# Performance work log

Measured on AMD Instinct MI355X. Metric: run time of the kernel, lower is better.

## Reference

```python
import math
import jax, jax.numpy as jnp
import numpy as np

EPS = 1e-5
B, S, D = 2, 2048, 2048
Z, HD, H, N = 512, 4096, 8, 8
ZH, VH = Z // H, HD // H  # 64, 512
GROUPS = 32


def timestep_norm(x, w, b):
    # cumulative (over time) group normalization; groups of dg channels
    dg = D // GROUPS
    xg = x.reshape(B, S, GROUPS, dg)
    s1 = jnp.cumsum(xg.sum(-1), axis=1)                 # [B,S,G]
    s2 = jnp.cumsum(jnp.square(xg).sum(-1), axis=1)     # [B,S,G]
    cnt = (jnp.arange(S, dtype=x.dtype) + 1.0) * dg
    mean = s1 / cnt[None, :, None]
    var = s2 / cnt[None, :, None] - jnp.square(mean)
    xn = (xg - mean[..., None]) * jax.lax.rsqrt(var[..., None] + EPS)
    return xn.reshape(B, S, D) * w + b


def cema(x, alpha, delta, theta, gamma, omega):
    # complex multi-head EMA: h_t = a*e^{i\theta} x_t + (1-a*d)*e^{i\theta} h_{t-1};
    # y_t = Re(gamma^H h_t) + omega * x_t    (real-arithmetic form, scan over time)
    p = jax.nn.sigmoid(alpha)                      # [D,N]
    qm = 1.0 - p * jax.nn.sigmoid(delta)           # [D,N]
    phase = jax.nn.sigmoid(theta)[:, None] * (2.0 * math.pi * (jnp.arange(N, dtype=x.dtype) + 1.0) / N)
    c, s = jnp.cos(phase), jnp.sin(phase)
    ur, ui = p * c, p * s
    qr, qi = qm * c, qm * s
    gr, gi = gamma[..., 0], gamma[..., 1]

    def step(h, xt):  # xt: [B,D]
        hr, hi = h
        nhr = qr * hr - qi * hi + ur * xt[..., None]
        nhi = qi * hr + qr * hi + ui * xt[..., None]
        y = jnp.sum(nhr * gr + nhi * gi, axis=-1)  # [B,D]
        return (nhr, nhi), y

    h0 = (jnp.zeros((B, D, N), x.dtype), jnp.zeros((B, D, N), x.dtype))
    _, ys = jax.lax.scan(step, h0, jnp.moveaxis(x, 1, 0))
    return jnp.moveaxis(ys, 0, 1) + x * omega


def rmsnorm(x, w=None):
    y = x * jax.lax.rsqrt(jnp.mean(jnp.square(x), axis=-1, keepdims=True) + EPS)
    return y if w is None else y * w


def apply_rotary(xq, xk, freqs):
    # xq/xk: [B,S,H,ZH]; freqs: [S, ZH//2, 2] (cos, sin)
    cos = freqs[None, :, None, :, 0]
    sin = freqs[None, :, None, :, 1]

    def rot(x):
        xr = x.reshape(*x.shape[:-1], ZH // 2, 2)
        re, im = xr[..., 0], xr[..., 1]
        out = jnp.stack([re * cos - im * sin, re * sin + im * cos], axis=-1)
        return out.reshape(x.shape)

    return rot(xq), rot(xk)


def setup_inputs():
    key = jax.random.key(0)
    ks = jax.random.split(key, 24)
    p = 0.02
    inp = {
        "x": jax.random.normal(ks[0], (B, S, D), jnp.float32),
        "tn_weight": 1.0 + p * jax.random.normal(ks[1], (D,), jnp.float32),
        "tn_bias": p * jax.random.normal(ks[2], (D,), jnp.float32),
        "ema_alpha": jax.random.normal(ks[3], (D, N), jnp.float32),
        "ema_delta": jax.random.normal(ks[4], (D, N), jnp.float32),
        "ema_theta": jax.random.normal(ks[5], (D,), jnp.float32),
        "ema_gamma": jax.random.normal(ks[6], (D, N, 2), jnp.float32) / math.sqrt(N),
        "ema_omega": p * jax.random.normal(ks[7], (D,), jnp.float32),
        "rms_weight": 1.0 + p * jax.random.normal(ks[8], (D,), jnp.float32),
        "wz_w": jax.random.normal(ks[9], (D, Z), jnp.float32) / math.sqrt(D),
        "wz_b": p * jax.random.normal(ks[10], (Z,), jnp.float32),
        "wv_w": jax.random.normal(ks[11], (D, HD), jnp.float32) / math.sqrt(D),
        "wv_b": p * jax.random.normal(ks[12], (HD,), jnp.float32),
        "wr_w": jax.random.normal(ks[13], (D, HD), jnp.float32) / math.sqrt(D),
        "wr_b": p * jax.random.normal(ks[14], (HD,), jnp.float32),
        "wh1_w": jax.random.normal(ks[15], (D, D), jnp.float32) / math.sqrt(D),
        "wh1_b": p * jax.random.normal(ks[16], (D,), jnp.float32),
        "wh2_w": jax.random.normal(ks[17], (HD, D), jnp.float32) / math.sqrt(HD),
        "attn_gamma": p * jax.random.normal(ks[18], (2, Z), jnp.float32),
        "attn_beta": p * jax.random.normal(ks[19], (2, Z), jnp.float32),
    }
    # rotary freqs (cos, sin) for head dim ZH
    inv = 1.0 / (10000.0 ** (np.arange(0, ZH, 2, dtype=np.float32) / ZH))
    ang = np.arange(S, dtype=np.float32)[:, None] * inv[None, :]
    inp["freqs_cis"] = jnp.asarray(np.stack([np.cos(ang), np.sin(ang)], axis=-1))
    return inp


def reference(x, freqs_cis, tn_weight, tn_bias, ema_alpha, ema_delta, ema_theta,
              ema_gamma, ema_omega, rms_weight, wz_w, wz_b, wv_w, wv_b, wr_w, wr_b,
              wh1_w, wh1_b, wh2_w, attn_gamma, attn_beta):
    residual = x
    out_tsn = timestep_norm(x, tn_weight, tn_bias)
    out_cema = cema(out_tsn, ema_alpha, ema_delta, ema_theta, ema_gamma, ema_omega)
    mx = rmsnorm(out_cema, rms_weight)

    z = mx @ wz_w + wz_b                              # [B,S,Z]
    z = rmsnorm(z.reshape(B, S, H, ZH)).reshape(B, S, Z)
    gamma = (attn_gamma + 1.0) / math.sqrt(ZH)        # [2,Z]
    z2 = z[:, :, None, :] * gamma + attn_beta         # [B,S,2,Z]
    q, k = z2[:, :, 0], z2[:, :, 1]

    v = jax.nn.silu(out_tsn @ wv_w + wv_b)            # [B,S,HD]
    r = jax.nn.silu(mx @ wr_w + wr_b)                 # [B,S,HD]

    qh = q.reshape(B, S, H, ZH)
    kh = k.reshape(B, S, H, ZH)
    vh = v.reshape(B, S, H, VH)
    qh, kh = apply_rotary(qh, kh, freqs_cis)

    # causal additive mask; scale 1.0 (folded into gamma)
    neg = jnp.finfo(jnp.float32).min
    mask = jnp.where(jnp.tril(jnp.ones((S, S), bool)), 0.0, neg).astype(jnp.float32)
    scores = jnp.einsum('bqhd,bkhd->bhqk', qh, kh) + mask
    probs = jax.nn.softmax(scores.astype(jnp.float32), axis=-1).astype(qh.dtype)
    attn = jnp.einsum('bhqk,bkhd->bqhd', probs, vh).reshape(B, S, HD)

    attn = attn * r
    h = (mx @ wh1_w + wh1_b) + attn @ wh2_w
    return h + residual
```

## Files before the change

### kernel.cpp

```cpp
#include <hip/hip_runtime.h>
#include <stdint.h>


typedef __bf16 bf16_t;
typedef bf16_t bf16x8 __attribute__((ext_vector_type(8)));
typedef float floatx4 __attribute__((ext_vector_type(4)));
typedef __attribute__((address_space(1))) unsigned int as1_uint;
typedef __attribute__((address_space(3))) unsigned int as3_uint;

static constexpr int kB = 2, kS = 2048, kD = 2048;
static constexpr int kZ = 512, kHD = 4096, kH = 8;
static constexpr int kG = 32;
static constexpr int kC = 64, kL = 32;

__device__ __forceinline__ void async16(void* lds, const void* g) {
  __builtin_amdgcn_global_load_lds((const as1_uint*)(size_t)g, (as3_uint*)lds, 16, 0, 0);
}

__device__ __forceinline__ float sigm(float x) { return 1.0f / (1.0f + expf(-x)); }

__global__ __launch_bounds__(256) void wtrans_kernel(const float* __restrict__ W,
                                                     bf16_t* __restrict__ Wt,
                                                     int K, int N, int ldWt,
                                                     int colOff) {
  __shared__ float tile[32][33];
  int n0 = blockIdx.x * 32, k0 = blockIdx.y * 32;
  int tx = threadIdx.x & 31, ty = threadIdx.x >> 5;
#pragma unroll
  for (int i = 0; i < 32; i += 8)
    tile[ty + i][tx] = W[(size_t)(k0 + ty + i) * N + n0 + tx];
  __syncthreads();
#pragma unroll
  for (int i = 0; i < 32; i += 8)
    Wt[(size_t)(n0 + ty + i) * ldWt + colOff + k0 + tx] = (bf16_t)tile[tx][ty + i];
}

__global__ __launch_bounds__(256) void tsn_sums(const float* __restrict__ x,
                                                float* __restrict__ g1,
                                                float* __restrict__ g2) {
  int bs = blockIdx.x, t = threadIdx.x;
  const float4* rp = (const float4*)(x + (size_t)bs * kD + t * 8);
  float4 a = rp[0], b = rp[1];
  float s1 = a.x + a.y + a.z + a.w + b.x + b.y + b.z + b.w;
  float s2 = a.x * a.x + a.y * a.y + a.z * a.z + a.w * a.w +
             b.x * b.x + b.y * b.y + b.z * b.z + b.w * b.w;
  s1 += __shfl_xor(s1, 1); s2 += __shfl_xor(s2, 1);
  s1 += __shfl_xor(s1, 2); s2 += __shfl_xor(s2, 2);
  s1 += __shfl_xor(s1, 4); s2 += __shfl_xor(s2, 4);
  if ((t & 7) == 0) {
    int g = t >> 3, b_ = bs >> 11, s = bs & 2047;
    size_t idx = ((size_t)b_ * kG + g) * kS + s;
    g1[idx] = s1; g2[idx] = s2;
  }
}

__global__ void tsn_scan(float* __restrict__ g1, float* __restrict__ g2) {
  int lane = threadIdx.x;
  size_t base = (size_t)blockIdx.x * kS;
  float c1 = 0.f, c2 = 0.f;
  for (int c = 0; c < kS / 64; ++c) {
    size_t idx = base + c * 64 + lane;
    float v1 = g1[idx], v2 = g2[idx];
#pragma unroll
    for (int off = 1; off < 64; off <<= 1) {
      float t1 = __shfl_up(v1, off), t2 = __shfl_up(v2, off);
      if (lane >= off) { v1 += t1; v2 += t2; }
    }
    v1 += c1; v2 += c2;
    g1[idx] = v1; g2[idx] = v2;
    c1 = __shfl(v1, 63); c2 = __shfl(v2, 63);
  }
}

__global__ __launch_bounds__(256) void tsn_norm(const float* __restrict__ x,
    const float* __restrict__ g1, const float* __restrict__ g2,
    const float* __restrict__ w, const float* __restrict__ bias,
    float* __restrict__ tsn, bf16_t* __restrict__ tsnb) {
  int bs = blockIdx.x, t = threadIdx.x;
  int b = bs >> 11, s = bs & 2047, g = t >> 3;
  float cnt = (float)(s + 1) * 64.0f;
  size_t gidx = ((size_t)b * kG + g) * kS + s;
  float mean = g1[gidx] / cnt;
  float inv = rsqrtf(g2[gidx] / cnt - mean * mean + 1e-5f);
  size_t base = (size_t)bs * kD + t * 8;
  float4 a = ((const float4*)(x + base))[0];
  float4 c = ((const float4*)(x + base))[1];
  float v[8] = {a.x, a.y, a.z, a.w, c.x, c.y, c.z, c.w};
  float4 w0 = ((const float4*)(w + t * 8))[0], w1 = ((const float4*)(w + t * 8))[1];
  float4 b0 = ((const float4*)(bias + t * 8))[0], b1 = ((const float4*)(bias + t * 8))[1];
  float wv[8] = {w0.x, w0.y, w0.z, w0.w, w1.x, w1.y, w1.z, w1.w};
  float bv[8] = {b0.x, b0.y, b0.z, b0.w, b1.x, b1.y, b1.z, b1.w};
  float r[8];
  bf16x8 ob;
#pragma unroll
  for (int i = 0; i < 8; ++i) {
    r[i] = (v[i] - mean) * inv * wv[i] + bv[i];
    ob[i] = (bf16_t)r[i];
  }
  ((float4*)(tsn + base))[0] = make_float4(r[0], r[1], r[2], r[3]);
  ((float4*)(tsn + base))[1] = make_float4(r[4], r[5], r[6], r[7]);
  *(bf16x8*)(tsnb + base) = ob;
}

__device__ __forceinline__ void cema_coeffs(const float* __restrict__ alpha,
    const float* __restrict__ delta, float st, int d,
    float (&qr)[8], float (&qi)[8], float (&ur)[8], float (&ui)[8]) {
  const float4* ap = (const float4*)(alpha + (size_t)d * 8);
  const float4* dp = (const float4*)(delta + (size_t)d * 8);
  float4 a0 = ap[0], a1 = ap[1], d0 = dp[0], d1 = dp[1];
  float av[8] = {a0.x, a0.y, a0.z, a0.w, a1.x, a1.y, a1.z, a1.w};
  float dv[8] = {d0.x, d0.y, d0.z, d0.w, d1.x, d1.y, d1.z, d1.w};
#pragma unroll
  for (int n = 0; n < 8; ++n) {
    float p = sigm(av[n]);
    float qm = 1.0f - p * sigm(dv[n]);
    float ph = st * (0.78539816339744831f * (float)(n + 1));
    float cs = cosf(ph), sn = sinf(ph);
    qr[n] = qm * cs; qi[n] = qm * sn;
    ur[n] = p * cs;  ui[n] = p * sn;
  }
}

__global__ __launch_bounds__(256) void cema_pass1(const float* __restrict__ tsn,
    const float* __restrict__ alpha, const float* __restrict__ delta,
    const float* __restrict__ theta, float2* __restrict__ hend) {
  int b = blockIdx.x >> 6, c = blockIdx.x & 63;
  int d = blockIdx.y * 256 + threadIdx.x;
  float st = sigm(theta[d]);
  float qr[8], qi[8], ur[8], ui[8];
  cema_coeffs(alpha, delta, st, d, qr, qi, ur, ui);
  float hr[8] = {0}, hi[8] = {0};
  const float* xp = tsn + ((size_t)b * kS + c * kL) * kD + d;
  for (int i = 0; i < kL; ++i) {
    float xt = xp[(size_t)i * kD];
#pragma unroll
    for (int n = 0; n < 8; ++n) {
      float tr = fmaf(qr[n], hr[n], fmaf(-qi[n], hi[n], ur[n] * xt));
      float ti = fmaf(qi[n], hr[n], fmaf(qr[n], hi[n], ui[n] * xt));
      hr[n] = tr; hi[n] = ti;
    }
  }
  float2* op = hend + (((size_t)(b * kC + c)) * kD + d) * 8;
#pragma unroll
  for (int n = 0; n < 8; ++n) op[n] = make_float2(hr[n], hi[n]);
}

__global__ __launch_bounds__(256) void cema_pass2(const float2* __restrict__ hend,
    const float* __restrict__ alpha, const float* __restrict__ delta,
    const float* __restrict__ theta, float2* __restrict__ hinit) {
  int tid = blockIdx.x * 256 + threadIdx.x;
  int n = tid & 7, d = (tid >> 3) & 2047, b = tid >> 14;
  int dn = d * 8 + n;
  float p = sigm(alpha[dn]);
  float qm = 1.0f - p * sigm(delta[dn]);
  float ph = sigm(theta[d]) * (0.78539816339744831f * (float)(n + 1));
  float ar = qm * cosf(ph), ai = qm * sinf(ph);
#pragma unroll
  for (int t = 0; t < 5; ++t) {
    float nr = ar * ar - ai * ai;
    ai = 2.0f * ar * ai;
    ar = nr;
  }
  float hr = 0.f, hi = 0.f;
  for (int c = 0; c < kC; ++c) {
    size_t idx = (((size_t)(b * kC + c)) * kD + d) * 8 + n;
    hinit[idx] = make_float2(hr, hi);
    float2 e = hend[idx];
    float nr = fmaf(ar, hr, fmaf(-ai, hi, e.x));
    float ni = fmaf(ai, hr, fmaf(ar, hi, e.y));
    hr = nr; hi = ni;
  }
}

__global__ __launch_bounds__(256) void cema_pass3(const float* __restrict__ tsn,
    const float* __restrict__ alpha, const float* __restrict__ delta,
    const float* __restrict__ theta, const float* __restrict__ gamma,
    const float* __restrict__ omega, const float2* __restrict__ hinit,
    float* __restrict__ outc) {
  int b = blockIdx.x >> 6, c = blockIdx.x & 63;
  int d = blockIdx.y * 256 + threadIdx.x;
  float st = sigm(theta[d]);
  float qr[8], qi[8], ur[8], ui[8];
  cema_coeffs(alpha, delta, st, d, qr, qi, ur, ui);
  float gr[8], gi[8];
  const float4* gp = (const float4*)(gamma + (size_t)d * 16);
#pragma unroll
  for (int m = 0; m < 4; ++m) {
    float4 g = gp[m];
    gr[m * 2] = g.x; gi[m * 2] = g.y; gr[m * 2 + 1] = g.z; gi[m * 2 + 1] = g.w;
  }
  float om = omega[d];
  float hr[8], hi[8];
  const float2* ip = hinit + (((size_t)(b * kC + c)) * kD + d) * 8;
#pragma unroll
  for (int n = 0; n < 8; ++n) { float2 h = ip[n]; hr[n] = h.x; hi[n] = h.y; }
  const float* xp = tsn + ((size_t)b * kS + c * kL) * kD + d;
  float* op = outc + ((size_t)b * kS + c * kL) * kD + d;
  for (int i = 0; i < kL; ++i) {
    float xt = xp[(size_t)i * kD];
    float y = 0.f;
#pragma unroll
    for (int n = 0; n < 8; ++n) {
      float tr = fmaf(qr[n], hr[n], fmaf(-qi[n], hi[n], ur[n] * xt));
      float ti = fmaf(qi[n], hr[n], fmaf(qr[n], hi[n], ui[n] * xt));
      hr[n] = tr; hi[n] = ti;
      y = fmaf(tr, gr[n], fmaf(ti, gi[n], y));
    }
    op[(size_t)i * kD] = fmaf(xt, om, y);
  }
}

__global__ __launch_bounds__(256) void rms_kernel(const float* __restrict__ in,
                                                  const float* __restrict__ w,
                                                  bf16_t* __restrict__ outb) {
  int bs = blockIdx.x, t = threadIdx.x;
  size_t base = (size_t)bs * kD + t * 8;
  float4 a = ((const float4*)(in + base))[0];
  float4 c = ((const float4*)(in + base))[1];
  float v[8] = {a.x, a.y, a.z, a.w, c.x, c.y, c.z, c.w};
  float ss = 0.f;
#pragma unroll
  for (int i = 0; i < 8; ++i) ss += v[i] * v[i];
#pragma unroll
  for (int off = 1; off < 64; off <<= 1) ss += __shfl_xor(ss, off);
  __shared__ float red[4];
  if ((t & 63) == 0) red[t >> 6] = ss;
  __syncthreads();
  ss = red[0] + red[1] + red[2] + red[3];
  float inv = rsqrtf(ss * (1.0f / 2048.0f) + 1e-5f);
  float4 w0 = ((const float4*)(w + t * 8))[0], w1 = ((const float4*)(w + t * 8))[1];
  float wv[8] = {w0.x, w0.y, w0.z, w0.w, w1.x, w1.y, w1.z, w1.w};
  bf16x8 ob;
#pragma unroll
  for (int i = 0; i < 8; ++i) ob[i] = (bf16_t)(v[i] * inv * wv[i]);
  *(bf16x8*)(outb + base) = ob;
}

__global__ __launch_bounds__(256) void zpost_kernel(const float* __restrict__ z,
    const float* __restrict__ ag, const float* __restrict__ ab,
    const float* __restrict__ freqs, bf16_t* __restrict__ q, bf16_t* __restrict__ k) {
  int bs = blockIdx.x, t = threadIdx.x;
  int b = bs >> 11, s = bs & 2047;
  int h = t >> 5, i = t & 31;
  const float* zr = z + (size_t)bs * kZ + h * 64;
  float re = zr[2 * i], im = zr[2 * i + 1];
  float ss = re * re + im * im;
#pragma unroll
  for (int off = 1; off < 32; off <<= 1) ss += __shfl_xor(ss, off);
  float inv = rsqrtf(ss * (1.0f / 64.0f) + 1e-5f);
  float zne = re * inv, zno = im * inv;
  const float rs = 0.125f;
  int ze = h * 64 + 2 * i, zo = ze + 1;
  float qe = zne * ((ag[ze] + 1.f) * rs) + ab[ze];
  float qo = zno * ((ag[zo] + 1.f) * rs) + ab[zo];
  float ke = zne * ((ag[kZ + ze] + 1.f) * rs) + ab[kZ + ze];
  float ko = zno * ((ag[kZ + zo] + 1.f) * rs) + ab[kZ + zo];
  float cs = freqs[((size_t)s * 32 + i) * 2 + 0];
  float sn = freqs[((size_t)s * 32 + i) * 2 + 1];
  size_t o = (((size_t)b * kH + h) * kS + s) * 64 + 2 * i;
  q[o]     = (bf16_t)(qe * cs - qo * sn);
  q[o + 1] = (bf16_t)(qe * sn + qo * cs);
  k[o]     = (bf16_t)(ke * cs - ko * sn);
  k[o + 1] = (bf16_t)(ke * sn + ko * cs);
}

__global__ __launch_bounds__(256) void gemm_fused3(
    const bf16_t* __restrict__ tsnb, const bf16_t* __restrict__ mx,
    const bf16_t* __restrict__ wvT, const bf16_t* __restrict__ wrT,
    const bf16_t* __restrict__ wzT, const float* __restrict__ wv_b,
    const float* __restrict__ wr_b, const float* __restrict__ wz_b,
    bf16_t* __restrict__ vTb, bf16_t* __restrict__ rb,
    float* __restrict__ zbuf) {
  __shared__ __align__(16) bf16_t sA[2][128 * 32];
  __shared__ __align__(16) bf16_t sB[2][128 * 32];
  const int bid = blockIdx.x;
  const bf16_t* A; const bf16_t* Bt; const float* bias;
  int N, epi, sub;
  if (bid < 1024)      { sub = bid;        A = tsnb; Bt = wvT; bias = wv_b; N = kHD; epi = 1; }
  else if (bid < 2048) { sub = bid - 1024; A = mx;   Bt = wrT; bias = wr_b; N = kHD; epi = 2; }
  else                 { sub = bid - 2048; A = mx;   Bt = wzT; bias = wz_b; N = kZ;  epi = 0; }
  const int m0 = (sub & 31) * 128, n0 = (sub >> 5) * 128;
  const int t = threadIdx.x;
  const int wave = t >> 6, lane = t & 63;
  const int quad = lane >> 4, l16 = lane & 15;
  const int wm = (wave >> 1) * 64, wn = (wave & 1) * 64;
  const int K = kD;

  floatx4 acc[4][4];
#pragma unroll
  for (int i = 0; i < 4; ++i)
#pragma unroll
    for (int j = 0; j < 4; ++j) acc[i][j] = (floatx4){0.f, 0.f, 0.f, 0.f};

  const int seg0 = wave * 64 + lane;
  const int seg1 = 256 + wave * 64 + lane;
  const int r0 = seg0 >> 2, c0 = (seg0 & 3) * 8;
  const int r1 = seg1 >> 2, c1 = (seg1 & 3) * 8;

  auto stage = [&](int buf, int kt) {
    async16(sA[buf] + (size_t)(wave * 64) * 8,       A + (size_t)(m0 + r0) * K + kt + c0);
    async16(sA[buf] + (size_t)(256 + wave * 64) * 8, A + (size_t)(m0 + r1) * K + kt + c1);
    async16(sB[buf] + (size_t)(wave * 64) * 8,       Bt + (size_t)(n0 + r0) * K + kt + c0);
    async16(sB[buf] + (size_t)(256 + wave * 64) * 8, Bt + (size_t)(n0 + r1) * K + kt + c1);
  };

  stage(0, 0);
  __syncthreads();

  const int nsteps = K >> 5;
  for (int st = 0; st < nsteps; ++st) {
    const int cur = st & 1;
    if (st + 1 < nsteps) stage(cur ^ 1, (st + 1) << 5);

    bf16x8 af[4], bfr[4];
#pragma unroll
    for (int i = 0; i < 4; ++i)
      af[i] = *(const bf16x8*)(sA[cur] + (wm + i * 16 + l16) * 32 + quad * 8);
#pragma unroll
    for (int j = 0; j < 4; ++j)
      bfr[j] = *(const bf16x8*)(sB[cur] + (wn + j * 16 + l16) * 32 + quad * 8);
#pragma unroll
    for (int i = 0; i < 4; ++i)
#pragma unroll
      for (int j = 0; j < 4; ++j)
        acc[i][j] = __builtin_amdgcn_mfma_f32_16x16x32_bf16(af[i], bfr[j], acc[i][j], 0, 0, 0);

    __syncthreads();
  }

#pragma unroll
  for (int i = 0; i < 4; ++i) {
#pragma unroll
    for (int j = 0; j < 4; ++j) {
#pragma unroll
      for (int r = 0; r < 4; ++r) {
        int row = m0 + wm + i * 16 + quad * 4 + r;
        int col = n0 + wn + j * 16 + l16;
        size_t idx = (size_t)row * N + col;
        float v = acc[i][j][r];
        if (epi == 0) {
          zbuf[idx] = v + bias[col];
        } else if (epi == 1) {
          v += bias[col];
          v = v / (1.f + __expf(-v));
          size_t vidx = ((size_t)(row >> 11) * kHD + col) * (size_t)kS + (row & 2047);
          vTb[vidx] = (bf16_t)v;
        } else {
          v += bias[col];
          v = v / (1.f + __expf(-v));
          rb[idx] = (bf16_t)v;
        }
      }
    }
  }
}

__global__ __launch_bounds__(256) void gemm_bt(const bf16_t* __restrict__ A1,
    int lda1, const bf16_t* __restrict__ A2, int lda2, int K1,
    const bf16_t* __restrict__ Bt, int M, int N, int K,
    const float* __restrict__ bias, const float* __restrict__ add1,
    float* __restrict__ outF) {
  __shared__ __align__(16) bf16_t sA[2][128 * 32];
  __shared__ __align__(16) bf16_t sB[2][128 * 32];
  const int t = threadIdx.x;
  const int wave = t >> 6, lane = t & 63;
  const int quad = lane >> 4, l16 = lane & 15;
  const int m0 = blockIdx.x * 128, n0 = blockIdx.y * 128;
  const int wm = (wave >> 1) * 64, wn = (wave & 1) * 64;

  floatx4 acc[4][4];
#pragma unroll
  for (int i = 0; i < 4; ++i)
#pragma unroll
    for (int j = 0; j < 4; ++j) acc[i][j] = (floatx4){0.f, 0.f, 0.f, 0.f};

  const int seg0 = wave * 64 + lane;
  const int seg1 = 256 + wave * 64 + lane;
  const int r0 = seg0 >> 2, c0 = (seg0 & 3) * 8;
  const int r1 = seg1 >> 2, c1 = (seg1 & 3) * 8;

  auto stage = [&](int buf, int kt) {
    const bf16_t* Ab; int ldab; int kk;
    if (kt < K1) { Ab = A1; ldab = lda1; kk = kt; }
    else         { Ab = A2; ldab = lda2; kk = kt - K1; }
    async16(sA[buf] + (size_t)(wave * 64) * 8,       Ab + (size_t)(m0 + r0) * ldab + kk + c0);
    async16(sA[buf] + (size_t)(256 + wave * 64) * 8, Ab + (size_t)(m0 + r1) * ldab + kk + c1);
    async16(sB[buf] + (size_t)(wave * 64) * 8,       Bt + (size_t)(n0 + r0) * K + kt + c0);
    async16(sB[buf] + (size_t)(256 + wave * 64) * 8, Bt + (size_t)(n0 + r1) * K + kt + c1);
  };

  stage(0, 0);
  __syncthreads();

  const int nsteps = K >> 5;
  for (int st = 0; st < nsteps; ++st) {
    const int cur = st & 1;
    if (st + 1 < nsteps) stage(cur ^ 1, (st + 1) << 5);

    bf16x8 af[4], bfr[4];
#pragma unroll
    for (int i = 0; i < 4; ++i)
      af[i] = *(const bf16x8*)(sA[cur] + (wm + i * 16 + l16) * 32 + quad * 8);
#pragma unroll
    for (int j = 0; j < 4; ++j)
      bfr[j] = *(const bf16x8*)(sB[cur] + (wn + j * 16 + l16) * 32 + quad * 8);
#pragma unroll
    for (int i = 0; i < 4; ++i)
#pragma unroll
      for (int j = 0; j < 4; ++j)
        acc[i][j] = __builtin_amdgcn_mfma_f32_16x16x32_bf16(af[i], bfr[j], acc[i][j], 0, 0, 0);

    __syncthreads();
  }

#pragma unroll
  for (int i = 0; i < 4; ++i) {
#pragma unroll
    for (int j = 0; j < 4; ++j) {
#pragma unroll
      for (int r = 0; r < 4; ++r) {
        int row = m0 + wm + i * 16 + quad * 4 + r;
        int col = n0 + wn + j * 16 + l16;
        size_t idx = (size_t)row * N + col;
        outF[idx] = acc[i][j][r] + bias[col] + add1[idx];
      }
    }
  }
}

__global__ __launch_bounds__(256) void attn_kernel(const bf16_t* __restrict__ qg,
    const bf16_t* __restrict__ kg, const bf16_t* __restrict__ vT,
    const bf16_t* __restrict__ rg, bf16_t* __restrict__ attnG) {
  const int bid = blockIdx.x;
  const int qt = (kS / 64 - 1) - (bid >> 5);
  const int bh = (bid >> 1) & 15;
  const int vs = bid & 1;
  const int b = bh >> 3, h = bh & 7;
  const int t = threadIdx.x;
  const int w = t >> 6, lane = t & 63;
  const int quad = lane >> 4, l16 = lane & 15;
  const int q0 = qt * 64;

  __shared__ __align__(16) bf16_t sP[2][64 * 64];
  __shared__ __align__(16) bf16_t sK[2][64 * 64];
  __shared__ float sM[64], sL[64], sAl[2][64];
  if (t < 64) { sM[t] = 0.f; sL[t] = 0.f; }

  const bf16_t* qbase = qg + ((size_t)bh * kS + q0) * 64;
  const bf16_t* kbase = kg + (size_t)bh * kS * 64;
  const bf16_t* vbase = vT + ((size_t)bh * 512 + vs * 256 + w * 64) * kS;

  auto stage_k = [&](bf16_t* dstbuf, int k0) {
#pragma unroll
    for (int half = 0; half < 2; ++half) {
      int seg = half * 256 + w * 64 + lane;
      int r = seg >> 3, cc = seg & 7;
      async16(dstbuf + (size_t)(half * 256 + w * 64) * 8,
              kbase + (size_t)(k0 + r) * 64 + (cc ^ (r & 7)) * 8);
    }
  };

  bf16x8 qfrag[2];
#pragma unroll
  for (int ks = 0; ks < 2; ++ks)
    qfrag[ks] = *(const bf16x8*)(qbase + (size_t)(w * 16 + l16) * 64 + ks * 32 + quad * 8);

  floatx4 oacc[4][4];
#pragma unroll
  for (int i = 0; i < 4; ++i)
#pragma unroll
    for (int j = 0; j < 4; ++j) oacc[i][j] = (floatx4){0.f, 0.f, 0.f, 0.f};

  stage_k(sK[0], 0);
  __syncthreads();

  for (int kt = 0; kt <= qt; ++kt) {
    const int k0 = kt * 64;
    const int pb = kt & 1;

    if (kt < qt) stage_k(sK[pb ^ 1], k0 + 64);

    bf16x8 vf[2][4];
#pragma unroll
    for (int ks = 0; ks < 2; ++ks)
#pragma unroll
      for (int nj = 0; nj < 4; ++nj)
        vf[ks][nj] = *(const bf16x8*)(vbase + (size_t)(nj * 16 + l16) * kS + k0 + ks * 32 + quad * 8);

    floatx4 sacc[4];
#pragma unroll
    for (int nt = 0; nt < 4; ++nt) sacc[nt] = (floatx4){0.f, 0.f, 0.f, 0.f};
#pragma unroll
    for (int ks = 0; ks < 2; ++ks)
#pragma unroll
      for (int nt = 0; nt < 4; ++nt) {
        int row = nt * 16 + l16;
        int ch = (ks * 4 + quad) ^ (row & 7);
        bf16x8 kf = *(const bf16x8*)(sK[pb] + row * 64 + ch * 8);
        sacc[nt] = __builtin_amdgcn_mfma_f32_16x16x32_bf16(qfrag[ks], kf, sacc[nt], 0, 0, 0);
      }
    if (kt == qt) {
#pragma unroll
      for (int nt = 0; nt < 4; ++nt)
#pragma unroll
        for (int r = 0; r < 4; ++r) {
          int sk = k0 + nt * 16 + l16;
          int qq = q0 + w * 16 + quad * 4 + r;
          if (sk > qq) sacc[nt][r] = -1e30f;
        }
    }

    float mo[4], mloc[4], lspec[4];
#pragma unroll
    for (int r = 0; r < 4; ++r) {
      mo[r] = sM[w * 16 + quad * 4 + r];
      mloc[r] = fmaxf(fmaxf(sacc[0][r], sacc[1][r]), fmaxf(sacc[2][r], sacc[3][r]));
    }
#pragma unroll
    for (int r = 0; r < 4; ++r) {
      float s = 0.f;
#pragma unroll
      for (int nt = 0; nt < 4; ++nt) {
        float e = __expf(sacc[nt][r] - mo[r]);
        sacc[nt][r] = e;
        s += e;
      }
      lspec[r] = s;
    }
#pragma unroll
    for (int off = 1; off < 16; off <<= 1)
#pragma unroll
      for (int r = 0; r < 4; ++r) {
        mloc[r] = fmaxf(mloc[r], __shfl_xor(mloc[r], off));
        lspec[r] += __shfl_xor(lspec[r], off);
      }
    float mnew[4], al[4];
#pragma unroll
    for (int r = 0; r < 4; ++r) {
      mnew[r] = fmaxf(mo[r], mloc[r]);
      al[r] = __expf(mo[r] - mnew[r]);
    }
    if (l16 == 0) {
#pragma unroll
      for (int r = 0; r < 4; ++r) {
        int row = w * 16 + quad * 4 + r;
        sM[row] = mnew[r];
        sL[row] = al[r] * (sL[row] + lspec[r]);
        sAl[pb][row] = al[r];
      }
    }
#pragma unroll
    for (int nt = 0; nt < 4; ++nt)
#pragma unroll
      for (int r = 0; r < 4; ++r) {
        int row = w * 16 + quad * 4 + r;
        sP[pb][row * 64 + ((nt * 16 + l16) ^ ((row & 7) << 3))] = (bf16_t)(sacc[nt][r] * al[r]);
      }

    __syncthreads();

#pragma unroll
    for (int mi = 0; mi < 4; ++mi)
#pragma unroll
      for (int r = 0; r < 4; ++r) {
        float a = sAl[pb][mi * 16 + quad * 4 + r];
#pragma unroll
        for (int nj = 0; nj < 4; ++nj) oacc[mi][nj][r] *= a;
      }
    __builtin_amdgcn_s_setprio(1);
#pragma unroll
    for (int ks = 0; ks < 2; ++ks) {
      bf16x8 pa[4];
#pragma unroll
      for (int mi = 0; mi < 4; ++mi) {
        int row = mi * 16 + l16;
        pa[mi] = *(const bf16x8*)(sP[pb] + row * 64 + ((ks * 32 + quad * 8) ^ ((row & 7) << 3)));
      }
#pragma unroll
      for (int nj = 0; nj < 4; ++nj)
#pragma unroll
        for (int mi = 0; mi < 4; ++mi)
          oacc[mi][nj] = __builtin_amdgcn_mfma_f32_16x16x32_bf16(pa[mi], vf[ks][nj], oacc[mi][nj], 0, 0, 0);
    }
    __builtin_amdgcn_s_setprio(0);
  }

#pragma unroll
  for (int mi = 0; mi < 4; ++mi)
#pragma unroll
    for (int r = 0; r < 4; ++r) {
      int srow = q0 + mi * 16 + quad * 4 + r;
      float linv = 1.0f / sL[mi * 16 + quad * 4 + r];
#pragma unroll
      for (int nj = 0; nj < 4; ++nj) {
        int hd = h * 512 + vs * 256 + w * 64 + nj * 16 + l16;
        size_t idx = ((size_t)b * kS + srow) * kHD + hd;
        float rv = (float)rg[idx];
        attnG[idx] = (bf16_t)(oacc[mi][nj][r] * linv * rv);
      }
    }
}

extern "C" void kernel_launch(void* const* d_in, const int* in_sizes, int n_in,
                              void* d_out, int out_size, void* d_ws, size_t ws_size,
                              hipStream_t stream) {
  const float* x      = (const float*)d_in[0];
  const float* tnw    = (const float*)d_in[1];
  const float* tnb    = (const float*)d_in[2];
  const float* ealpha = (const float*)d_in[3];
  const float* edelta = (const float*)d_in[4];
  const float* etheta = (const float*)d_in[5];
  const float* egamma = (const float*)d_in[6];
  const float* eomega = (const float*)d_in[7];
  const float* rmsw   = (const float*)d_in[8];
  const float* wz_w   = (const float*)d_in[9];
  const float* wz_b   = (const float*)d_in[10];
  const float* wv_w   = (const float*)d_in[11];
  const float* wv_b   = (const float*)d_in[12];
  const float* wr_w   = (const float*)d_in[13];
  const float* wr_b   = (const float*)d_in[14];
  const float* wh1_w  = (const float*)d_in[15];
  const float* wh1_b  = (const float*)d_in[16];
  const float* wh2_w  = (const float*)d_in[17];
  const float* ag     = (const float*)d_in[18];
  const float* ab     = (const float*)d_in[19];
  const float* freqs  = (const float*)d_in[20];
  float* out = (float*)d_out;

  char* ws = (char*)d_ws;
  size_t off = 0;
  auto alloc = [&](size_t bytes) -> void* {
    void* p = ws + off;
    off += (bytes + 255) & ~(size_t)255;
    return p;
  };
  float*  tsn  = (float*)alloc(8388608ull * 4);
  bf16_t* tsnb = (bf16_t*)alloc(8388608ull * 2);
  float*  g1   = (float*)alloc(131072ull * 4);
  float*  g2   = (float*)alloc(131072ull * 4);
  float*  cema = (float*)alloc(8388608ull * 4);
  bf16_t* mx   = (bf16_t*)alloc(8388608ull * 2);
  bf16_t* wzT  = (bf16_t*)alloc(1048576ull * 2);
  bf16_t* wvT  = (bf16_t*)alloc(8388608ull * 2);
  bf16_t* wrT  = (bf16_t*)alloc(8388608ull * 2);
  bf16_t* whcT = (bf16_t*)alloc(12582912ull * 2);
  float*  zbuf = (float*)alloc(2097152ull * 4);
  bf16_t* qb   = (bf16_t*)alloc(2097152ull * 2);
  bf16_t* kb   = (bf16_t*)alloc(2097152ull * 2);
  bf16_t* rb   = (bf16_t*)alloc(16777216ull * 2);
  bf16_t* aG   = (bf16_t*)alloc(16777216ull * 2);
  bf16_t* vTb  = (bf16_t*)tsn;
  float*  h1   = cema;
  float2* hend  = (float2*)rb;
  float2* hinit = (float2*)aG;
  (void)h1;

  wtrans_kernel<<<dim3(kZ / 32, kD / 32), 256, 0, stream>>>(wz_w, wzT, kD, kZ, kD, 0);
  wtrans_kernel<<<dim3(kHD / 32, kD / 32), 256, 0, stream>>>(wv_w, wvT, kD, kHD, kD, 0);
  wtrans_kernel<<<dim3(kHD / 32, kD / 32), 256, 0, stream>>>(wr_w, wrT, kD, kHD, kD, 0);
  wtrans_kernel<<<dim3(kD / 32, kD / 32), 256, 0, stream>>>(wh1_w, whcT, kD, kD, 6144, 0);
  wtrans_kernel<<<dim3(kD / 32, kHD / 32), 256, 0, stream>>>(wh2_w, whcT, kHD, kD, 6144, kD);

  tsn_sums<<<kB * kS, 256, 0, stream>>>(x, g1, g2);
  tsn_scan<<<kB * kG, 64, 0, stream>>>(g1, g2);
  tsn_norm<<<kB * kS, 256, 0, stream>>>(x, g1, g2, tnw, tnb, tsn, tsnb);

  cema_pass1<<<dim3(kB * kC, kD / 256), 256, 0, stream>>>(tsn, ealpha, edelta,
                                                          etheta, hend);
  cema_pass2<<<kB * kD * 8 / 256, 256, 0, stream>>>(hend, ealpha, edelta,
                                                    etheta, hinit);
  cema_pass3<<<dim3(kB * kC, kD / 256), 256, 0, stream>>>(tsn, ealpha, edelta,
      etheta, egamma, eomega, hinit, cema);
  rms_kernel<<<kB * kS, 256, 0, stream>>>(cema, rmsw, mx);

  const int M = kB * kS;
  gemm_fused3<<<dim3(2176), 256, 0, stream>>>(tsnb, mx, wvT, wrT, wzT,
      wv_b, wr_b, wz_b, vTb, rb, zbuf);
  zpost_kernel<<<kB * kS, 256, 0, stream>>>(zbuf, ag, ab, freqs, qb, kb);
  attn_kernel<<<dim3(1024), 256, 0, stream>>>(qb, kb, vTb, rb, aG);
  gemm_bt<<<dim3(M / 128, kD / 128), 256, 0, stream>>>(mx, kD, aG, kHD, kD,
      whcT, M, kD, 6144, wh1_b, x, out);
  (void)in_sizes; (void)n_in; (void)out_size; (void)ws_size;
}
```

Measured before the change: 872.4 us.

## Overlap mx@wh1 GEMM with attention by co-launching in one kernel

The final GEMM is split in two. The independent mx@wh1 part (K=2048), plus bias and residual, now runs as 512 extra blocks appended to the attention launch, so it fills idle CUs while the causally imbalanced attention blocks run. A second GEMM over the attention output (K=4096) then adds onto the stored partial. This costs an extra fp32 write and read of the partial buffer and a separate launch for the second GEMM.

```diff
diff --git a/kernel.cpp b/kernel.cpp
--- a/kernel.cpp
+++ b/kernel.cpp
@@ -355,10 +355,254 @@
   }
 }
 
-__global__ __launch_bounds__(256) void gemm_bt(const bf16_t* __restrict__ A1,
-    int lda1, const bf16_t* __restrict__ A2, int lda2, int K1,
-    const bf16_t* __restrict__ Bt, int M, int N, int K,
-    const float* __restrict__ bias, const float* __restrict__ add1,
+__global__ __launch_bounds__(256) void fused_attn_wh1(
+    const bf16_t* __restrict__ qg, const bf16_t* __restrict__ kg,
+    const bf16_t* __restrict__ vT, const bf16_t* __restrict__ rg,
+    bf16_t* __restrict__ attnG,
+    const bf16_t* __restrict__ mx, const bf16_t* __restrict__ whcT,
+    const float* __restrict__ wh1_b, const float* __restrict__ x,
+    float* __restrict__ Pw0) {
+  __shared__ __align__(16) char smem[33792];
+  const int bid = blockIdx.x;
+  const int t = threadIdx.x;
+  const int w = t >> 6, lane = t & 63;
+  const int quad = lane >> 4, l16 = lane & 15;
+
+  if (bid >= 1024) {
+    bf16_t* sA = (bf16_t*)smem;
+    bf16_t* sB = (bf16_t*)(smem + 16384);
+    const int sub = bid - 1024;
+    const int m0 = (sub & 31) * 128, n0 = (sub >> 5) * 128;
+    const int wm = (w >> 1) * 64, wn = (w & 1) * 64;
+    const int N = kD, K = kD, ldB = 6144;
+
+    floatx4 acc[4][4];
+#pragma unroll
+    for (int i = 0; i < 4; ++i)
+#pragma unroll
+      for (int j = 0; j < 4; ++j) acc[i][j] = (floatx4){0.f, 0.f, 0.f, 0.f};
+
+    const int seg0 = w * 64 + lane;
+    const int seg1 = 256 + w * 64 + lane;
+    const int r0 = seg0 >> 2, c0 = (seg0 & 3) * 8;
+    const int r1 = seg1 >> 2, c1 = (seg1 & 3) * 8;
+
+    auto stage = [&](int buf, int kt) {
+      bf16_t* sAb = sA + buf * 4096;
+      bf16_t* sBb = sB + buf * 4096;
+      async16(sAb + (size_t)(w * 64) * 8,       mx + (size_t)(m0 + r0) * K + kt + c0);
+      async16(sAb + (size_t)(256 + w * 64) * 8, mx + (size_t)(m0 + r1) * K + kt + c1);
+      async16(sBb + (size_t)(w * 64) * 8,       whcT + (size_t)(n0 + r0) * ldB + kt + c0);
+      async16(sBb + (size_t)(256 + w * 64) * 8, whcT + (size_t)(n0 + r1) * ldB + kt + c1);
+    };
+
+    stage(0, 0);
+    __syncthreads();
+
+    const int nsteps = K >> 5;
+    for (int st = 0; st < nsteps; ++st) {
+      const int cur = st & 1;
+      if (st + 1 < nsteps) stage(cur ^ 1, (st + 1) << 5);
+
+      bf16x8 af[4], bfr[4];
+#pragma unroll
+      for (int i = 0; i < 4; ++i)
+        af[i] = *(const bf16x8*)(sA + cur * 4096 + (wm + i * 16 + l16) * 32 + quad * 8);
+#pragma unroll
+      for (int j = 0; j < 4; ++j)
+        bfr[j] = *(const bf16x8*)(sB + cur * 4096 + (wn + j * 16 + l16) * 32 + quad * 8);
+#pragma unroll
+      for (int i = 0; i < 4; ++i)
+#pragma unroll
+        for (int j = 0; j < 4; ++j)
+          acc[i][j] = __builtin_amdgcn_mfma_f32_16x16x32_bf16(af[i], bfr[j], acc[i][j], 0, 0, 0);
+
+      __syncthreads();
+    }
+
+#pragma unroll
+    for (int i = 0; i < 4; ++i)
+#pragma unroll
+      for (int j = 0; j < 4; ++j)
+#pragma unroll
+        for (int r = 0; r < 4; ++r) {
+          int row = m0 + wm + i * 16 + quad * 4 + r;
+          int col = n0 + wn + j * 16 + l16;
+          size_t idx = (size_t)row * N + col;
+          Pw0[idx] = acc[i][j][r] + wh1_b[col] + x[idx];
+        }
+    return;
+  }
+
+  bf16_t* sP = (bf16_t*)smem;
+  bf16_t* sK = (bf16_t*)(smem + 16384);
+  float* sM  = (float*)(smem + 32768);
+  float* sL  = (float*)(smem + 33024);
+  float* sAl = (float*)(smem + 33280);
+  const int qt = (kS / 64 - 1) - (bid >> 5);
+  const int bh = (bid >> 1) & 15;
+  const int vs = bid & 1;
+  const int b = bh >> 3, h = bh & 7;
+  const int q0 = qt * 64;
+  if (t < 64) { sM[t] = 0.f; sL[t] = 0.f; }
+
+  const bf16_t* qbase = qg + ((size_t)bh * kS + q0) * 64;
+  const bf16_t* kbase = kg + (size_t)bh * kS * 64;
+  const bf16_t* vbase = vT + ((size_t)bh * 512 + vs * 256 + w * 64) * kS;
+
+  auto stage_k = [&](bf16_t* dstbuf, int k0) {
+#pragma unroll
+    for (int half = 0; half < 2; ++half) {
+      int seg = half * 256 + w * 64 + lane;
+      int r = seg >> 3, cc = seg & 7;
+      async16(dstbuf + (size_t)(half * 256 + w * 64) * 8,
+              kbase + (size_t)(k0 + r) * 64 + (cc ^ (r & 7)) * 8);
+    }
+  };
+
+  bf16x8 qfrag[2];
+#pragma unroll
+  for (int ks = 0; ks < 2; ++ks)
+    qfrag[ks] = *(const bf16x8*)(qbase + (size_t)(w * 16 + l16) * 64 + ks * 32 + quad * 8);
+
+  floatx4 oacc[4][4];
+#pragma unroll
+  for (int i = 0; i < 4; ++i)
+#pragma unroll
+    for (int j = 0; j < 4; ++j) oacc[i][j] = (floatx4){0.f, 0.f, 0.f, 0.f};
+
+  stage_k(sK, 0);
+  __syncthreads();
+
+  for (int kt = 0; kt <= qt; ++kt) {
+    const int k0 = kt * 64;
+    const int pb = kt & 1;
+
+    if (kt < qt) stage_k(sK + (pb ^ 1) * 4096, k0 + 64);
+
+    bf16x8 vf[2][4];
+#pragma unroll
+    for (int ks = 0; ks < 2; ++ks)
+#pragma unroll
+      for (int nj = 0; nj < 4; ++nj)
+        vf[ks][nj] = *(const bf16x8*)(vbase + (size_t)(nj * 16 + l16) * kS + k0 + ks * 32 + quad * 8);
+
+    floatx4 sacc[4];
+#pragma unroll
+    for (int nt = 0; nt < 4; ++nt) sacc[nt] = (floatx4){0.f, 0.f, 0.f, 0.f};
+#pragma unroll
+    for (int ks = 0; ks < 2; ++ks)
+#pragma unroll
+      for (int nt = 0; nt < 4; ++nt) {
+        int row = nt * 16 + l16;
+        int ch = (ks * 4 + quad) ^ (row & 7);
+        bf16x8 kf = *(const bf16x8*)(sK + pb * 4096 + row * 64 + ch * 8);
+        sacc[nt] = __builtin_amdgcn_mfma_f32_16x16x32_bf16(qfrag[ks], kf, sacc[nt], 0, 0, 0);
+      }
+    if (kt == qt) {
+#pragma unroll
+      for (int nt = 0; nt < 4; ++nt)
+#pragma unroll
+        for (int r = 0; r < 4; ++r) {
+          int sk = k0 + nt * 16 + l16;
+          int qq = q0 + w * 16 + quad * 4 + r;
+          if (sk > qq) sacc[nt][r] = -1e30f;
+        }
+    }
+
+    float mo[4], mloc[4], lspec[4];
+#pragma unroll
+    for (int r = 0; r < 4; ++r) {
+      mo[r] = sM[w * 16 + quad * 4 + r];
+      mloc[r] = fmaxf(fmaxf(sacc[0][r], sacc[1][r]), fmaxf(sacc[2][r], sacc[3][r]));
+    }
+#pragma unroll
+    for (int r = 0; r < 4; ++r) {
+      float s = 0.f;
+#pragma unroll
+      for (int nt = 0; nt < 4; ++nt) {
+        float e = __expf(sacc[nt][r] - mo[r]);
+        sacc[nt][r] = e;
+        s += e;
+      }
+      lspec[r] = s;
+    }
+#pragma unroll
+    for (int off = 1; off < 16; off <<= 1)
+#pragma unroll
+      for (int r = 0; r < 4; ++r) {
+        mloc[r] = fmaxf(mloc[r], __shfl_xor(mloc[r], off));
+        lspec[r] += __shfl_xor(lspec[r], off);
+      }
+    float mnew[4], al[4];
+#pragma unroll
+    for (int r = 0; r < 4; ++r) {
+      mnew[r] = fmaxf(mo[r], mloc[r]);
+      al[r] = __expf(mo[r] - mnew[r]);
+    }
+    if (l16 == 0) {
+#pragma unroll
+      for (int r = 0; r < 4; ++r) {
+        int row = w * 16 + quad * 4 + r;
+        sM[row] = mnew[r];
+        sL[row] = al[r] * (sL[row] + lspec[r]);
+        sAl[pb * 64 + row] = al[r];
+      }
+    }
+#pragma unroll
+    for (int nt = 0; nt < 4; ++nt)
+#pragma unroll
+      for (int r = 0; r < 4; ++r) {
+        int row = w * 16 + quad * 4 + r;
+        sP[pb * 4096 + row * 64 + ((nt * 16 + l16) ^ ((row & 7) << 3))] = (bf16_t)(sacc[nt][r] * al[r]);
+      }
+
+    __syncthreads();
+
+#pragma unroll
+    for (int mi = 0; mi < 4; ++mi)
+#pragma unroll
+      for (int r = 0; r < 4; ++r) {
+        float a = sAl[pb * 64 + mi * 16 + quad * 4 + r];
+#pragma unroll
+        for (int nj = 0; nj < 4; ++nj) oacc[mi][nj][r] *= a;
+      }
+    __builtin_amdgcn_s_setprio(1);
+#pragma unroll
+    for (int ks = 0; ks < 2; ++ks) {
+      bf16x8 pa[4];
+#pragma unroll
+      for (int mi = 0; mi < 4; ++mi) {
+        int row = mi * 16 + l16;
+        pa[mi] = *(const bf16x8*)(sP + pb * 4096 + row * 64 + ((ks * 32 + quad * 8) ^ ((row & 7) << 3)));
+      }
+#pragma unroll
+      for (int nj = 0; nj < 4; ++nj)
+#pragma unroll
+        for (int mi = 0; mi < 4; ++mi)
+          oacc[mi][nj] = __builtin_amdgcn_mfma_f32_16x16x32_bf16(pa[mi], vf[ks][nj], oacc[mi][nj], 0, 0, 0);
+    }
+    __builtin_amdgcn_s_setprio(0);
+  }
+
+#pragma unroll
+  for (int mi = 0; mi < 4; ++mi)
+#pragma unroll
+    for (int r = 0; r < 4; ++r) {
+      int srow = q0 + mi * 16 + quad * 4 + r;
+      float linv = 1.0f / sL[mi * 16 + quad * 4 + r];
+#pragma unroll
+      for (int nj = 0; nj < 4; ++nj) {
+        int hd = h * 512 + vs * 256 + w * 64 + nj * 16 + l16;
+        size_t idx = ((size_t)b * kS + srow) * kHD + hd;
+        float rv = (float)rg[idx];
+        attnG[idx] = (bf16_t)(oacc[mi][nj][r] * linv * rv);
+      }
+    }
+}
+
+__global__ __launch_bounds__(256) void gemm_final(const bf16_t* __restrict__ aG,
+    const bf16_t* __restrict__ whcT, const float* __restrict__ Pw0,
     float* __restrict__ outF) {
   __shared__ __align__(16) bf16_t sA[2][128 * 32];
   __shared__ __align__(16) bf16_t sB[2][128 * 32];
@@ -367,6 +611,7 @@
   const int quad = lane >> 4, l16 = lane & 15;
   const int m0 = blockIdx.x * 128, n0 = blockIdx.y * 128;
   const int wm = (wave >> 1) * 64, wn = (wave & 1) * 64;
+  const int N = kD, K = kHD, lda = kHD, ldB = 6144, cOff = 2048;
 
   floatx4 acc[4][4];
 #pragma unroll
@@ -380,13 +625,10 @@
   const int r1 = seg1 >> 2, c1 = (seg1 & 3) * 8;
 
   auto stage = [&](int buf, int kt) {
-    const bf16_t* Ab; int ldab; int kk;
-    if (kt < K1) { Ab = A1; ldab = lda1; kk = kt; }
-    else         { Ab = A2; ldab = lda2; kk = kt - K1; }
-    async16(sA[buf] + (size_t)(wave * 64) * 8,       Ab + (size_t)(m0 + r0) * ldab + kk + c0);
-    async16(sA[buf] + (size_t)(256 + wave * 64) * 8, Ab + (size_t)(m0 + r1) * ldab + kk + c1);
-    async16(sB[buf] + (size_t)(wave * 64) * 8,       Bt + (size_t)(n0 + r0) * K + kt + c0);
-    async16(sB[buf] + (size_t)(256 + wave * 64) * 8, Bt + (size_t)(n0 + r1) * K + kt + c1);
+    async16(sA[buf] + (size_t)(wave * 64) * 8,       aG + (size_t)(m0 + r0) * lda + kt + c0);
+    async16(sA[buf] + (size_t)(256 + wave * 64) * 8, aG + (size_t)(m0 + r1) * lda + kt + c1);
+    async16(sB[buf] + (size_t)(wave * 64) * 8,       whcT + (size_t)(n0 + r0) * ldB + cOff + kt + c0);
+    async16(sB[buf] + (size_t)(256 + wave * 64) * 8, whcT + (size_t)(n0 + r1) * ldB + cOff + kt + c1);
   };
 
   stage(0, 0);
@@ -414,191 +656,16 @@
   }
 
 #pragma unroll
-  for (int i = 0; i < 4; ++i) {
-#pragma unroll
-    for (int j = 0; j < 4; ++j) {
+  for (int i = 0; i < 4; ++i)
+#pragma unroll
+    for (int j = 0; j < 4; ++j)
 #pragma unroll
       for (int r = 0; r < 4; ++r) {
         int row = m0 + wm + i * 16 + quad * 4 + r;
         int col = n0 + wn + j * 16 + l16;
         size_t idx = (size_t)row * N + col;
-        outF[idx] = acc[i][j][r] + bias[col] + add1[idx];
-      }
-    }
-  }
-}
-
-__global__ __launch_bounds__(256) void attn_kernel(const bf16_t* __restrict__ qg,
-    const bf16_t* __restrict__ kg, const bf16_t* __restrict__ vT,
-    const bf16_t* __restrict__ rg, bf16_t* __restrict__ attnG) {
-  const int bid = blockIdx.x;
-  const int qt = (kS / 64 - 1) - (bid >> 5);
-  const int bh = (bid >> 1) & 15;
-  const int vs = bid & 1;
-  const int b = bh >> 3, h = bh & 7;
-  const int t = threadIdx.x;
-  const int w = t >> 6, lane = t & 63;
-  const int quad = lane >> 4, l16 = lane & 15;
-  const int q0 = qt * 64;
-
-  __shared__ __align__(16) bf16_t sP[2][64 * 64];
-  __shared__ __align__(16) bf16_t sK[2][64 * 64];
-  __shared__ float sM[64], sL[64], sAl[2][64];
-  if (t < 64) { sM[t] = 0.f; sL[t] = 0.f; }
-
-  const bf16_t* qbase = qg + ((size_t)bh * kS + q0) * 64;
-  const bf16_t* kbase = kg + (size_t)bh * kS * 64;
-  const bf16_t* vbase = vT + ((size_t)bh * 512 + vs * 256 + w * 64) * kS;
-
-  auto stage_k = [&](bf16_t* dstbuf, int k0) {
-#pragma unroll
-    for (int half = 0; half < 2; ++half) {
-      int seg = half * 256 + w * 64 + lane;
-      int r = seg >> 3, cc = seg & 7;
-      async16(dstbuf + (size_t)(half * 256 + w * 64) * 8,
-              kbase + (size_t)(k0 + r) * 64 + (cc ^ (r & 7)) * 8);
-    }
-  };
-
-  bf16x8 qfrag[2];
-#pragma unroll
-  for (int ks = 0; ks < 2; ++ks)
-    qfrag[ks] = *(const bf16x8*)(qbase + (size_t)(w * 16 + l16) * 64 + ks * 32 + quad * 8);
-
-  floatx4 oacc[4][4];
-#pragma unroll
-  for (int i = 0; i < 4; ++i)
-#pragma unroll
-    for (int j = 0; j < 4; ++j) oacc[i][j] = (floatx4){0.f, 0.f, 0.f, 0.f};
-
-  stage_k(sK[0], 0);
-  __syncthreads();
-
-  for (int kt = 0; kt <= qt; ++kt) {
-    const int k0 = kt * 64;
-    const int pb = kt & 1;
-
-    if (kt < qt) stage_k(sK[pb ^ 1], k0 + 64);
-
-    bf16x8 vf[2][4];
-#pragma unroll
-    for (int ks = 0; ks < 2; ++ks)
-#pragma unroll
-      for (int nj = 0; nj < 4; ++nj)
-        vf[ks][nj] = *(const bf16x8*)(vbase + (size_t)(nj * 16 + l16) * kS + k0 + ks * 32 + quad * 8);
-
-    floatx4 sacc[4];
-#pragma unroll
-    for (int nt = 0; nt < 4; ++nt) sacc[nt] = (floatx4){0.f, 0.f, 0.f, 0.f};
-#pragma unroll
-    for (int ks = 0; ks < 2; ++ks)
-#pragma unroll
-      for (int nt = 0; nt < 4; ++nt) {
-        int row = nt * 16 + l16;
-        int ch = (ks * 4 + quad) ^ (row & 7);
-        bf16x8 kf = *(const bf16x8*)(sK[pb] + row * 64 + ch * 8);
-        sacc[nt] = __builtin_amdgcn_mfma_f32_16x16x32_bf16(qfrag[ks], kf, sacc[nt], 0, 0, 0);
-      }
-    if (kt == qt) {
-#pragma unroll
-      for (int nt = 0; nt < 4; ++nt)
-#pragma unroll
-        for (int r = 0; r < 4; ++r) {
-          int sk = k0 + nt * 16 + l16;
-          int qq = q0 + w * 16 + quad * 4 + r;
-          if (sk > qq) sacc[nt][r] = -1e30f;
-        }
-    }
-
-    float mo[4], mloc[4], lspec[4];
-#pragma unroll
-    for (int r = 0; r < 4; ++r) {
-      mo[r] = sM[w * 16 + quad * 4 + r];
-      mloc[r] = fmaxf(fmaxf(sacc[0][r], sacc[1][r]), fmaxf(sacc[2][r], sacc[3][r]));
-    }
-#pragma unroll
-    for (int r = 0; r < 4; ++r) {
-      float s = 0.f;
-#pragma unroll
-      for (int nt = 0; nt < 4; ++nt) {
-        float e = __expf(sacc[nt][r] - mo[r]);
-        sacc[nt][r] = e;
-        s += e;
-      }
-      lspec[r] = s;
-    }
-#pragma unroll
-    for (int off = 1; off < 16; off <<= 1)
-#pragma unroll
-      for (int r = 0; r < 4; ++r) {
-        mloc[r] = fmaxf(mloc[r], __shfl_xor(mloc[r], off));
-        lspec[r] += __shfl_xor(lspec[r], off);
-      }
-    float mnew[4], al[4];
-#pragma unroll
-    for (int r = 0; r < 4; ++r) {
-      mnew[r] = fmaxf(mo[r], mloc[r]);
-      al[r] = __expf(mo[r] - mnew[r]);
-    }
-    if (l16 == 0) {
-#pragma unroll
-      for (int r = 0; r < 4; ++r) {
-        int row = w * 16 + quad * 4 + r;
-        sM[row] = mnew[r];
-        sL[row] = al[r] * (sL[row] + lspec[r]);
-        sAl[pb][row] = al[r];
-      }
-    }
-#pragma unroll
-    for (int nt = 0; nt < 4; ++nt)
-#pragma unroll
-      for (int r = 0; r < 4; ++r) {
-        int row = w * 16 + quad * 4 + r;
-        sP[pb][row * 64 + ((nt * 16 + l16) ^ ((row & 7) << 3))] = (bf16_t)(sacc[nt][r] * al[r]);
-      }
-
-    __syncthreads();
-
-#pragma unroll
-    for (int mi = 0; mi < 4; ++mi)
-#pragma unroll
-      for (int r = 0; r < 4; ++r) {
-        float a = sAl[pb][mi * 16 + quad * 4 + r];
-#pragma unroll
-        for (int nj = 0; nj < 4; ++nj) oacc[mi][nj][r] *= a;
-      }
-    __builtin_amdgcn_s_setprio(1);
-#pragma unroll
-    for (int ks = 0; ks < 2; ++ks) {
-      bf16x8 pa[4];
-#pragma unroll
-      for (int mi = 0; mi < 4; ++mi) {
-        int row = mi * 16 + l16;
-        pa[mi] = *(const bf16x8*)(sP[pb] + row * 64 + ((ks * 32 + quad * 8) ^ ((row & 7) << 3)));
-      }
-#pragma unroll
-      for (int nj = 0; nj < 4; ++nj)
-#pragma unroll
-        for (int mi = 0; mi < 4; ++mi)
-          oacc[mi][nj] = __builtin_amdgcn_mfma_f32_16x16x32_bf16(pa[mi], vf[ks][nj], oacc[mi][nj], 0, 0, 0);
-    }
-    __builtin_amdgcn_s_setprio(0);
-  }
-
-#pragma unroll
-  for (int mi = 0; mi < 4; ++mi)
-#pragma unroll
-    for (int r = 0; r < 4; ++r) {
-      int srow = q0 + mi * 16 + quad * 4 + r;
-      float linv = 1.0f / sL[mi * 16 + quad * 4 + r];
-#pragma unroll
-      for (int nj = 0; nj < 4; ++nj) {
-        int hd = h * 512 + vs * 256 + w * 64 + nj * 16 + l16;
-        size_t idx = ((size_t)b * kS + srow) * kHD + hd;
-        float rv = (float)rg[idx];
-        attnG[idx] = (bf16_t)(oacc[mi][nj][r] * linv * rv);
-      }
-    }
+        outF[idx] = acc[i][j][r] + Pw0[idx];
+      }
 }
 
 extern "C" void kernel_launch(void* const* d_in, const int* in_sizes, int n_in,
@@ -650,10 +717,9 @@
   bf16_t* rb   = (bf16_t*)alloc(16777216ull * 2);
   bf16_t* aG   = (bf16_t*)alloc(16777216ull * 2);
   bf16_t* vTb  = (bf16_t*)tsn;
-  float*  h1   = cema;
+  float*  Pw0  = cema;
   float2* hend  = (float2*)rb;
   float2* hinit = (float2*)aG;
-  (void)h1;
 
   wtrans_kernel<<<dim3(kZ / 32, kD / 32), 256, 0, stream>>>(wz_w, wzT, kD, kZ, kD, 0);
   wtrans_kernel<<<dim3(kHD / 32, kD / 32), 256, 0, stream>>>(wv_w, wvT, kD, kHD, kD, 0);
@@ -677,8 +743,8 @@
   gemm_fused3<<<dim3(2176), 256, 0, stream>>>(tsnb, mx, wvT, wrT, wzT,
       wv_b, wr_b, wz_b, vTb, rb, zbuf);
   zpost_kernel<<<kB * kS, 256, 0, stream>>>(zbuf, ag, ab, freqs, qb, kb);
-  attn_kernel<<<dim3(1024), 256, 0, stream>>>(qb, kb, vTb, rb, aG);
-  gemm_bt<<<dim3(M / 128, kD / 128), 256, 0, stream>>>(mx, kD, aG, kHD, kD,
-      whcT, M, kD, 6144, wh1_b, x, out);
+  fused_attn_wh1<<<dim3(1536), 256, 0, stream>>>(qb, kb, vTb, rb, aG,
+      mx, whcT, wh1_b, x, Pw0);
+  gemm_final<<<dim3(M / 128, kD / 128), 256, 0, stream>>>(aG, whcT, Pw0, out);
   (void)in_sizes; (void)n_in; (void)out_size; (void)ws_size;
 }
```

Result: slower. 941.0 us (+7.9%).
